# Optimization experiments

Hardware: AMD Instinct MI355X
Metric: run time of the kernel (lower is better)

Reference implementation:

```python
import jax, jax.numpy as jnp
import numpy as np

H = 2048  # hid_dim
D = 2048  # input_dim (gru input size)
L = 256   # input_len


def setup_inputs() -> dict:
    key = jax.random.key(0)
    ks = jax.random.split(key, 16)
    s_pre = 1.0 / np.sqrt(7)
    s_gru = 1.0 / np.sqrt(H)
    s_out = 1.0 / np.sqrt(H)
    return {
        "timepoints": jax.random.uniform(ks[0], (L, 1), jnp.float32),
        "pk_data": jax.random.normal(ks[1], (L, 1), jnp.float32),
        "input_len": L,
        "emb_patient": 5,
        "drug_route": jax.random.uniform(ks[2], (1,), jnp.float32),
        "dose": jax.random.uniform(ks[3], (1,), jnp.float32),
        "smiles": jax.random.normal(ks[4], (1, H), jnp.float32),
        "tf_mask": jax.random.randint(ks[5], (L,), 0, 2, jnp.int32),
        "emb_table": jax.random.normal(ks[6], (8, 3), jnp.float32),
        "W_pre": jax.random.uniform(ks[7], (D, 7), jnp.float32, -s_pre, s_pre),
        "b_pre": jax.random.uniform(ks[8], (D,), jnp.float32, -s_pre, s_pre),
        "W_ih": jax.random.uniform(ks[9], (3 * H, D), jnp.float32, -s_gru, s_gru),
        "W_hh": jax.random.uniform(ks[10], (3 * H, H), jnp.float32, -s_gru, s_gru),
        "b_ih": jax.random.uniform(ks[11], (3 * H,), jnp.float32, -s_gru, s_gru),
        "b_hh": jax.random.uniform(ks[12], (3 * H,), jnp.float32, -s_gru, s_gru),
        "W_out": jax.random.uniform(ks[13], (1, H), jnp.float32, -s_out, s_out),
        "b_out": jax.random.uniform(ks[14], (1,), jnp.float32, -s_out, s_out),
    }


def _gru_cell(x, h, W_ih, W_hh, b_ih, b_hh):
    # PyTorch GRUCell math. x: [D], h: [H]
    gi = W_ih @ x + b_ih            # [3H]
    gh = W_hh @ h + b_hh            # [3H]
    i_r, i_z, i_n = jnp.split(gi, 3)
    h_r, h_z, h_n = jnp.split(gh, 3)
    r = jax.nn.sigmoid(i_r + h_r)
    z = jax.nn.sigmoid(i_z + h_z)
    n = jnp.tanh(i_n + r * h_n)
    return (1.0 - z) * n + z * h


def reference(timepoints, pk_data, input_len, emb_patient, drug_route, dose,
              smiles, tf_mask, emb_table, W_pre, b_pre, W_ih, W_hh, b_ih,
              b_hh, W_out, b_out):
    add_info = jnp.concatenate([emb_table[emb_patient], drug_route])  # [4]
    h0 = smiles[0]          # [H]
    pk0 = pk_data[0]        # [1]

    def step(carry, xs):
        pk, h = carry
        tp_prev, pk_teach, tf = xs
        x7 = jnp.concatenate([pk, tp_prev, dose, add_info])  # [7]
        x = W_pre @ x7 + b_pre                               # [D]
        h = _gru_cell(x, h, W_ih, W_hh, b_ih, b_hh)          # [H]
        pred = W_out @ h + b_out                             # [1]
        pk_next = jnp.where(tf == 1, pred, pk_teach)
        return (pk_next, h), pred

    xs = (timepoints[:-1], pk_data[1:], tf_mask[1:])
    _, preds = jax.lax.scan(step, (pk0, h0), xs)             # [L-1, 1]
    outputs = jnp.concatenate([pk0[None, :], preds], axis=0)  # [L, 1]
    return outputs
```

## Files before the change

kernel.cpp:

```cpp
#include <hip/hip_runtime.h>
#include <math.h>

#define Hdim 2048
#define Ldim 256
#define NBLK 256
#define TPB  1024
#define JPB  8
#define NREP 8

typedef unsigned long long u64;

#define WS_HP 0

__global__ __launch_bounds__(TPB, 4) void gru_all(
    const float* __restrict__ Whh,  const float* __restrict__ bhh,
    const float* __restrict__ Wout, const float* __restrict__ bout,
    const float* __restrict__ tps,  const float* __restrict__ pkdata,
    const int*   __restrict__ tf,   const float* __restrict__ smiles,
    const float* __restrict__ Wp,   const float* __restrict__ bpre,
    const float* __restrict__ Wih,  const float* __restrict__ bih,
    const float* __restrict__ dose, const float* __restrict__ route,
    const float* __restrict__ emb,  const int* __restrict__ pat,
    float* __restrict__ ws, float* __restrict__ out)
{
    const int b    = blockIdx.x;
    const int tid  = threadIdx.x;
    const int k    = tid & 127;
    const int g    = tid >> 7;
    const int wv   = tid >> 6;
    const int lane = tid & 63;
    const int j    = b*JPB + g;
    const int rep  = b & 7;

    __shared__ float su[Hdim];
    __shared__ float sh_h[Hdim];
    __shared__ float sred[16][3];
    __shared__ float swp[2][16];
    __shared__ float sA[24], sT[24], sC[24];
    __shared__ float s_tp[Ldim];
    __shared__ float s_pkd[Ldim];
    __shared__ int   s_tf[Ldim];

    unsigned* hq = (unsigned*)(ws + WS_HP);

    for (int i = tid; i < Ldim; i += TPB) {
        s_tp[i]  = tps[i];
        s_pkd[i] = pkdata[i];
        s_tf[i]  = tf[i];
    }

    {
        float d = dose[0], rt = route[0];
        int p = pat[0];
        float e0 = emb[p*3+0], e1 = emb[p*3+1], e2 = emb[p*3+2];
        for (int i = tid; i < Hdim; i += TPB) {
            const float* wr = Wp + i*7;
            su[i] = d*wr[2] + e0*wr[3] + e1*wr[4] + e2*wr[5] + rt*wr[6] + bpre[i];
        }
    }

    float4 w[3][4];
    #pragma unroll
    for (int r = 0; r < 3; ++r) {
        const float* base = Whh + (size_t)(j + r*Hdim) * Hdim;
        #pragma unroll
        for (int c = 0; c < 4; ++c)
            w[r][c] = *(const float4*)(base + c*512 + k*4);
    }

    const int i0 = tid * 2;
    const float wo0 = Wout[i0], wo1 = Wout[i0 + 1];
    const float bo = bout[0];

    __syncthreads();

    #pragma unroll
    for (int pass = 0; pass < 2; ++pass) {
        int ri = wv + pass*16;
        if (ri < 24) {
            int grow = (ri >> 3)*Hdim + b*JPB + (ri & 7);
            const float* wr = Wih + (size_t)grow * Hdim;
            float s0 = 0.f, s1 = 0.f, s2 = 0.f;
            #pragma unroll
            for (int c = 0; c < 8; ++c) {
                int col = c*256 + lane*4;
                float4 wv4 = *(const float4*)(wr + col);
                float4 uv4 = *(const float4*)(su + col);
                s0 += wv4.x*Wp[(col+0)*7+0] + wv4.y*Wp[(col+1)*7+0]
                    + wv4.z*Wp[(col+2)*7+0] + wv4.w*Wp[(col+3)*7+0];
                s1 += wv4.x*Wp[(col+0)*7+1] + wv4.y*Wp[(col+1)*7+1]
                    + wv4.z*Wp[(col+2)*7+1] + wv4.w*Wp[(col+3)*7+1];
                s2 += wv4.x*uv4.x + wv4.y*uv4.y + wv4.z*uv4.z + wv4.w*uv4.w;
            }
            #pragma unroll
            for (int off = 32; off >= 1; off >>= 1) {
                s0 += __shfl_down(s0, off, 64);
                s1 += __shfl_down(s1, off, 64);
                s2 += __shfl_down(s2, off, 64);
            }
            if (lane == 0) {
                sA[ri] = s0;
                sT[ri] = s1;
                sC[ri] = s2 + bih[grow];
            }
        }
    }
    __syncthreads();

    float apk_r=0, apk_z=0, apk_n=0, atp_r=0, atp_z=0, atp_n=0,
          cvt_r=0, cvt_z=0, cvt_n=0, br=0, bz=0, bn=0, hprev=0;
    if (wv == 0) {
        float hinit = 0.f;
        if (lane < JPB) {
            int jj = b*JPB + lane;
            apk_r = sA[lane]; apk_z = sA[8+lane]; apk_n = sA[16+lane];
            atp_r = sT[lane]; atp_z = sT[8+lane]; atp_n = sT[16+lane];
            cvt_r = sC[lane]; cvt_z = sC[8+lane]; cvt_n = sC[16+lane];
            br = bhh[jj]; bz = bhh[jj + Hdim]; bn = bhh[jj + 2*Hdim];
            hprev = smiles[jj];
            hinit = hprev;
        }
        float hv = __shfl(hinit, lane & 7);
        unsigned w0 = (__float_as_uint(hv) & 0xFFFFFF00u);
        __hip_atomic_store(hq + (size_t)(lane >> 3)*Hdim + b*JPB + (lane & 7), w0,
                           __ATOMIC_RELAXED, __HIP_MEMORY_SCOPE_AGENT);
        if (b == 0 && lane == 0) out[0] = pkdata[0];
    }

    for (int t = 0; t < Ldim - 1; ++t) {
        const int pr_ = t & 1;
        const unsigned* hin = hq + (size_t)(pr_*NREP + rep)*Hdim;
        const unsigned tt = (unsigned)t & 0xFFu;

        u64 q;
        for (;;) {
            q = __hip_atomic_load((const u64*)(hin + i0),
                                  __ATOMIC_RELAXED, __HIP_MEMORY_SCOPE_AGENT);
            if (((unsigned)q & 0xFFu) == tt &&
                ((unsigned)(q >> 32) & 0xFFu) == tt) break;
        }
        float h0 = __uint_as_float((unsigned)q         & 0xFFFFFF00u);
        float h1 = __uint_as_float((unsigned)(q >> 32) & 0xFFFFFF00u);
        sh_h[i0]     = h0;
        sh_h[i0 + 1] = h1;

        float wpart = wo0*h0 + wo1*h1;
        #pragma unroll
        for (int off = 32; off >= 1; off >>= 1) wpart += __shfl_down(wpart, off, 64);
        if (lane == 0) swp[pr_][wv] = wpart;
        __syncthreads();

        float prd = 0.f, pzd = 0.f, pnd = 0.f;
        #pragma unroll
        for (int c = 0; c < 4; ++c) {
            float4 hv4 = *(const float4*)(sh_h + c*512 + k*4);
            prd += w[0][c].x*hv4.x + w[0][c].y*hv4.y + w[0][c].z*hv4.z + w[0][c].w*hv4.w;
            pzd += w[1][c].x*hv4.x + w[1][c].y*hv4.y + w[1][c].z*hv4.z + w[1][c].w*hv4.w;
            pnd += w[2][c].x*hv4.x + w[2][c].y*hv4.y + w[2][c].z*hv4.z + w[2][c].w*hv4.w;
        }
        #pragma unroll
        for (int off = 32; off >= 1; off >>= 1) {
            prd += __shfl_down(prd, off, 64);
            pzd += __shfl_down(pzd, off, 64);
            pnd += __shfl_down(pnd, off, 64);
        }
        if (lane == 0) { sred[wv][0] = prd; sred[wv][1] = pzd; sred[wv][2] = pnd; }
        __syncthreads();

        if (wv == 0) {
            float s = (lane < 16) ? swp[pr_][lane] : 0.f;
            s += __shfl_down(s, 8, 64);
            s += __shfl_down(s, 4, 64);
            s += __shfl_down(s, 2, 64);
            s += __shfl_down(s, 1, 64);
            float pred = __shfl(s, 0) + bo;
            float pk = (t == 0) ? s_pkd[0] : ((s_tf[t] == 1) ? pred : s_pkd[t]);
            if (b == 0 && lane == 0 && t > 0) out[t] = pred;
            float hvnew = 0.f;
            if (lane < JPB) {
                float dotr = sred[2*lane][0] + sred[2*lane+1][0];
                float dotz = sred[2*lane][1] + sred[2*lane+1][1];
                float dotn = sred[2*lane][2] + sred[2*lane+1][2];
                float tp  = s_tp[t];
                float gr  = apk_r*pk + atp_r*tp + cvt_r + dotr + br;
                float gz  = apk_z*pk + atp_z*tp + cvt_z + dotz + bz;
                float gin = apk_n*pk + atp_n*tp + cvt_n;
                float r = 1.0f / (1.0f + expf(-gr));
                float z = 1.0f / (1.0f + expf(-gz));
                float n = tanhf(gin + r*(dotn + bn));
                hvnew = (1.0f - z)*n + z*hprev;
                hprev = hvnew;
            }
            float hv = __shfl(hvnew, lane & 7);
            unsigned wpk = (__float_as_uint(hv) & 0xFFFFFF00u)
                         | ((unsigned)(t + 1) & 0xFFu);
            __hip_atomic_store(hq + (size_t)(((pr_^1)*NREP) + (lane >> 3))*Hdim
                                   + b*JPB + (lane & 7), wpk,
                               __ATOMIC_RELAXED, __HIP_MEMORY_SCOPE_AGENT);
        }
    }

    if (b == 0) {
        const unsigned* hin = hq + (size_t)((((Ldim - 1) & 1))*NREP + 0)*Hdim;
        const unsigned tt = (unsigned)(Ldim - 1) & 0xFFu;
        u64 q;
        for (;;) {
            q = __hip_atomic_load((const u64*)(hin + i0),
                                  __ATOMIC_RELAXED, __HIP_MEMORY_SCOPE_AGENT);
            if (((unsigned)q & 0xFFu) == tt &&
                ((unsigned)(q >> 32) & 0xFFu) == tt) break;
        }
        float h0 = __uint_as_float((unsigned)q         & 0xFFFFFF00u);
        float h1 = __uint_as_float((unsigned)(q >> 32) & 0xFFFFFF00u);
        float wpart = wo0*h0 + wo1*h1;
        #pragma unroll
        for (int off = 32; off >= 1; off >>= 1) wpart += __shfl_down(wpart, off, 64);
        if (lane == 0) swp[1][wv] = wpart;
        __syncthreads();
        if (wv == 0) {
            float s = (lane < 16) ? swp[1][lane] : 0.f;
            s += __shfl_down(s, 8, 64);
            s += __shfl_down(s, 4, 64);
            s += __shfl_down(s, 2, 64);
            s += __shfl_down(s, 1, 64);
            if (lane == 0) out[Ldim - 1] = s + bo;
        }
    }
}

extern "C" void kernel_launch(void* const* d_in, const int* in_sizes, int n_in,
                              void* d_out, int out_size, void* d_ws, size_t ws_size,
                              hipStream_t stream)
{
    const float* tps    = (const float*)d_in[0];
    const float* pkdata = (const float*)d_in[1];
    const int*   pat    = (const int*)  d_in[3];
    const float* route  = (const float*)d_in[4];
    const float* dose   = (const float*)d_in[5];
    const float* smiles = (const float*)d_in[6];
    const int*   tfm    = (const int*)  d_in[7];
    const float* emb    = (const float*)d_in[8];
    const float* Wp     = (const float*)d_in[9];
    const float* bpre   = (const float*)d_in[10];
    const float* Wih    = (const float*)d_in[11];
    const float* Whh    = (const float*)d_in[12];
    const float* bih    = (const float*)d_in[13];
    const float* bhh    = (const float*)d_in[14];
    const float* Wout   = (const float*)d_in[15];
    const float* bout   = (const float*)d_in[16];
    float* out = (float*)d_out;
    float* ws  = (float*)d_ws;

    hipLaunchKernelGGL(gru_all, dim3(NBLK), dim3(TPB), 0, stream,
                       Whh, bhh, Wout, bout, tps, pkdata, tfm, smiles,
                       Wp, bpre, Wih, bih, dose, route, emb, pat, ws, out);
}
```

Before: 1.012 ms.

## Gate per-step h reads on a compact per-block step-flag array

Result: slower. 1.218 ms (+20.4%).

```diff
diff --git a/kernel.cpp b/kernel.cpp
--- a/kernel.cpp
+++ b/kernel.cpp
@@ -9,8 +9,17 @@
 #define NREP 8
 
 typedef unsigned long long u64;
-
-#define WS_HP 0
+typedef int i32x4 __attribute__((ext_vector_type(4)));
+
+#define PAYLOAD_WORDS (2*NREP*Hdim)
+
+__device__ __forceinline__ i32x4 ld16_cohr(const int* p) {
+    i32x4 v;
+    asm volatile("global_load_dwordx4 %0, %1, off sc0 sc1\n\t"
+                 "s_waitcnt vmcnt(0)"
+                 : "=v"(v) : "v"(p) : "memory");
+    return v;
+}
 
 __global__ __launch_bounds__(TPB, 4) void gru_all(
     const float* __restrict__ Whh,  const float* __restrict__ bhh,
@@ -41,7 +50,8 @@
     __shared__ float s_pkd[Ldim];
     __shared__ int   s_tf[Ldim];
 
-    unsigned* hq = (unsigned*)(ws + WS_HP);
+    unsigned* hq = (unsigned*)ws;
+    int*      sq = (int*)(hq + PAYLOAD_WORDS);
 
     for (int i = tid; i < Ldim; i += TPB) {
         s_tp[i]  = tps[i];
@@ -124,6 +134,9 @@
         unsigned w0 = (__float_as_uint(hv) & 0xFFFFFF00u);
         __hip_atomic_store(hq + (size_t)(lane >> 3)*Hdim + b*JPB + (lane & 7), w0,
                            __ATOMIC_RELAXED, __HIP_MEMORY_SCOPE_AGENT);
+        if (lane < NREP)
+            __hip_atomic_store(sq + lane*256 + b, 0,
+                               __ATOMIC_RELAXED, __HIP_MEMORY_SCOPE_AGENT);
         if (b == 0 && lane == 0) out[0] = pkdata[0];
     }
 
@@ -131,6 +144,15 @@
         const int pr_ = t & 1;
         const unsigned* hin = hq + (size_t)(pr_*NREP + rep)*Hdim;
         const unsigned tt = (unsigned)t & 0xFFu;
+
+        if (wv == 0) {
+            const int* sp = sq + rep*256 + lane*4;
+            for (;;) {
+                i32x4 s4 = ld16_cohr(sp);
+                if (__all(s4.x >= t && s4.y >= t && s4.z >= t && s4.w >= t)) break;
+            }
+        }
+        __syncthreads();
 
         u64 q;
         for (;;) {
@@ -197,12 +219,24 @@
             __hip_atomic_store(hq + (size_t)(((pr_^1)*NREP) + (lane >> 3))*Hdim
                                    + b*JPB + (lane & 7), wpk,
                                __ATOMIC_RELAXED, __HIP_MEMORY_SCOPE_AGENT);
+            if (lane < NREP)
+                __hip_atomic_store(sq + lane*256 + b, t + 1,
+                                   __ATOMIC_RELAXED, __HIP_MEMORY_SCOPE_AGENT);
         }
     }
 
     if (b == 0) {
-        const unsigned* hin = hq + (size_t)((((Ldim - 1) & 1))*NREP + 0)*Hdim;
-        const unsigned tt = (unsigned)(Ldim - 1) & 0xFFu;
+        const int tF = Ldim - 1;
+        if (wv == 0) {
+            const int* sp = sq + 0*256 + lane*4;
+            for (;;) {
+                i32x4 s4 = ld16_cohr(sp);
+                if (__all(s4.x >= tF && s4.y >= tF && s4.z >= tF && s4.w >= tF)) break;
+            }
+        }
+        __syncthreads();
+        const unsigned* hin = hq + (size_t)((tF & 1)*NREP + 0)*Hdim;
+        const unsigned tt = (unsigned)tF & 0xFFu;
         u64 q;
         for (;;) {
             q = __hip_atomic_load((const u64*)(hin + i0),
```
